# Kernel optimization log

Measured on AMD Instinct MI355X. Metric: run time of the kernel, lower is better.

Reference implementation:

```python
import jax, jax.numpy as jnp
import numpy as np

S_IN = 10.0   # sharpness_inside
S_OUT = 10.0  # sharpness_outside
NEG_FILL = -100.0  # value written outside the ellipsoid mask


def _quat_to_rot(q):
    # q: (B, M, 4) -> (B, M, 3, 3)
    q = q / jnp.linalg.norm(q, axis=-1, keepdims=True)
    w, x, y, z = q[..., 0], q[..., 1], q[..., 2], q[..., 3]
    R = jnp.stack([
        1 - 2 * (y * y + z * z), 2 * (x * y - w * z), 2 * (x * z + w * y),
        2 * (x * y + w * z), 1 - 2 * (x * x + z * z), 2 * (y * z - w * x),
        2 * (x * z - w * y), 2 * (y * z + w * x), 1 - 2 * (x * x + y * y),
    ], axis=-1)
    return R.reshape(q.shape[:-1] + (3, 3))


def setup_inputs() -> dict:
    key = jax.random.key(0)
    ks = jax.random.split(key, 12)
    B, N, P, M, C, H = 2, 256, 32, 16, 128, 256

    def lin(k, fan_in, shape):
        return (jax.random.normal(k, shape, jnp.float32) / np.sqrt(fan_in)).astype(jnp.float32)

    return {
        'ray_points': jax.random.normal(ks[0], (B, N, P, 3), jnp.float32),
        'translations': 0.5 * jax.random.normal(ks[1], (B, M, 3), jnp.float32),
        'rotations': jax.random.normal(ks[2], (B, M, 4), jnp.float32),
        'scale': 0.2 + 0.8 * jax.random.uniform(ks[3], (B, M, 3), jnp.float32),
        'part_shape_features': jax.random.normal(ks[4], (B, M, C), jnp.float32),
        'Wp': lin(ks[5], 3, (3, H)),   'bp': jnp.zeros((H,), jnp.float32),
        'Wc': lin(ks[6], C, (C, H)),   'bc': jnp.zeros((H,), jnp.float32),
        'W1': lin(ks[7], H, (H, H)),   'b1': jnp.zeros((H,), jnp.float32),
        'W2': lin(ks[8], H, (H, H)),   'b2': jnp.zeros((H,), jnp.float32),
        'Wout': lin(ks[9], H, (H, 1)), 'bout': jnp.zeros((1,), jnp.float32),
    }


def reference(ray_points, translations, rotations, scale, part_shape_features,
              Wp, bp, Wc, bc, W1, b1, W2, b2, Wout, bout):
    B, N, P, _ = ray_points.shape
    M = translations.shape[1]
    pts = ray_points.reshape(B, N * P, 3)

    # transform_to_primitives_centric_system: R @ (x - t)
    Xc = pts[:, :, None, :] - translations[:, None, :, :]          # (B, Np, M, 3)
    R = _quat_to_rot(rotations)                                    # (B, M, 3, 3)
    Xt = jnp.einsum('bmij,bnmj->bnmi', R, Xc)                      # (B, Np, M, 3)

    # inside_outside_function_ellipsoid: F = sum((x/a)^2)
    F_ell = jnp.sum((Xt / scale[:, None, :, :]) ** 2, axis=-1)     # (B, Np, M)
    mask = F_ell <= 1.0

    # MiniOccupancyNet: fc_p + per-block conditioning + resnet block + fc_out
    net = jnp.einsum('bnmd,dh->bnmh', Xt, Wp) + bp                 # (B, Np, M, H)
    cond = jnp.einsum('bmc,ch->bmh', part_shape_features, Wc) + bc # (B, M, H)
    net = net + cond[:, None, :, :]
    dx = jax.nn.relu(net) @ W1 + b1
    dx = jax.nn.relu(dx) @ W2 + b2
    net = net + dx
    occ = (jax.nn.relu(net) @ Wout + bout)[..., 0]                 # (B, Np, M)

    # masked gather-compute-scatter == dense compute + fill -100 outside mask
    F = jnp.where(mask, occ, NEG_FILL)

    # apply_sigmoid_to_inside_outside_function: piecewise sharpness
    sharp = jnp.where(F > 0, S_IN, S_OUT)
    implicit = jax.nn.sigmoid(sharp * F)                           # (B, Np, M)
    return implicit.reshape(B, N, P, M)
```

## Files before the change

### kernel.cpp

```cpp
#include <hip/hip_runtime.h>
#include <hip/hip_fp16.h>
#include <math.h>

#define B_   2
#define N_   256
#define P_   32
#define M_   16
#define C_   128
#define H_   256
#define NP_  (N_ * P_)
#define ROWS_ (B_ * NP_ * M_)
#define HALF_ (ROWS_ / 2)
#define TM_  64
#define LDA_ (H_ + 8)
#define MROWS_ 1024
#define MBLK_ (ROWS_ / MROWS_)

typedef _Float16 half8 __attribute__((ext_vector_type(8)));
typedef float f32x4 __attribute__((ext_vector_type(4)));

__global__ __launch_bounds__(256)
void prep_mask_k(const float* __restrict__ W1, const float* __restrict__ W2,
                 _Float16* __restrict__ Wt1, _Float16* __restrict__ Wt2,
                 const float* __restrict__ psf, const float* __restrict__ Wc,
                 const float* __restrict__ bc, const float* __restrict__ Wp,
                 const float* __restrict__ bp, _Float16* __restrict__ B0t,
                 const float* __restrict__ pts, const float* __restrict__ trans,
                 const float* __restrict__ rots, const float* __restrict__ scal,
                 int* __restrict__ cnt, int* __restrict__ wl,
                 float* __restrict__ out) {
    __shared__ float t[64][65];
    const int tid = threadIdx.x;

    if (blockIdx.x < 32) {
        const int id = blockIdx.x;
        const float* W = (id & 1) ? W2 : W1;
        _Float16* Wt = (id & 1) ? Wt2 : Wt1;
        const int tile = id >> 1, I = tile >> 2, J = tile & 3;
        const int r = tid >> 6, c = tid & 63;
        #pragma unroll
        for (int p = 0; p < 16; ++p)
            t[p * 4 + r][c] = W[(I * 64 + p * 4 + r) * H_ + J * 64 + c];
        __syncthreads();
        #pragma unroll
        for (int p = 0; p < 16; ++p)
            Wt[(J * 64 + p * 4 + r) * H_ + I * 64 + c] = (_Float16)t[c][p * 4 + r];
        return;
    }
    if (blockIdx.x < 64) {
        const int bm = blockIdx.x - 32;
        const int b = bm >> 4, m = bm & 15;
        const int h = tid;
        const float* p = psf + bm * C_;
        float acc = bc[h];
        for (int c = 0; c < C_; ++c) acc += p[c] * Wc[c * H_ + h];
        _Float16* dst = B0t + (b * H_ + h) * 32;
        dst[3 + m] = (_Float16)(acc + bp[h]);
        if (m == 0) {
            dst[0] = (_Float16)Wp[h];
            dst[1] = (_Float16)Wp[H_ + h];
            dst[2] = (_Float16)Wp[2 * H_ + h];
            #pragma unroll
            for (int k = 19; k < 32; ++k) dst[k] = (_Float16)0.0f;
        }
        return;
    }

    float (*sR)[9] = (float (*)[9])&t[0][0];
    float (*sT)[3] = (float (*)[3])&t[4][0];
    float (*sS)[3] = (float (*)[3])&t[8][0];
    __shared__ int sBuf[MROWS_];
    __shared__ int sCnt;
    __shared__ int sBase;

    const int base = (blockIdx.x - 64) * MROWS_;
    const int b    = base >> 17;

    if (tid == 0) sCnt = 0;
    if (tid < M_) {
        const int m = tid;
        const float* q = rots + (b * M_ + m) * 4;
        float w = q[0], x = q[1], y = q[2], z = q[3];
        float nrm = sqrtf(w * w + x * x + y * y + z * z);
        w /= nrm; x /= nrm; y /= nrm; z /= nrm;
        sR[m][0] = 1.0f - 2.0f * (y * y + z * z);
        sR[m][1] = 2.0f * (x * y - w * z);
        sR[m][2] = 2.0f * (x * z + w * y);
        sR[m][3] = 2.0f * (x * y + w * z);
        sR[m][4] = 1.0f - 2.0f * (x * x + z * z);
        sR[m][5] = 2.0f * (y * z - w * x);
        sR[m][6] = 2.0f * (x * z - w * y);
        sR[m][7] = 2.0f * (y * z + w * x);
        sR[m][8] = 1.0f - 2.0f * (x * x + y * y);
        const float* tp = trans + (b * M_ + m) * 3;
        sT[m][0] = tp[0]; sT[m][1] = tp[1]; sT[m][2] = tp[2];
        const float* sp = scal + (b * M_ + m) * 3;
        sS[m][0] = sp[0]; sS[m][1] = sp[1]; sS[m][2] = sp[2];
    }
    __syncthreads();

    const int m = tid & (M_ - 1);
    #pragma unroll
    for (int r = 0; r < 4; ++r) {
        const int row = base + r * 256 + tid;
        const int gp  = row >> 4;
        float fe;
        {
            #pragma clang fp contract(off)
            const float* p = pts + gp * 3;
            float x0 = p[0] - sT[m][0];
            float x1 = p[1] - sT[m][1];
            float x2 = p[2] - sT[m][2];
            float t0 = sR[m][0] * x0 + sR[m][1] * x1 + sR[m][2] * x2;
            float t1 = sR[m][3] * x0 + sR[m][4] * x1 + sR[m][5] * x2;
            float t2 = sR[m][6] * x0 + sR[m][7] * x1 + sR[m][8] * x2;
            float v0 = t0 / sS[m][0];
            float v1 = t1 / sS[m][1];
            float v2 = t2 / sS[m][2];
            fe = v0 * v0 + v1 * v1 + v2 * v2;
        }
        if (fe <= 1.0f) {
            const int pos = atomicAdd(&sCnt, 1);
            sBuf[pos] = row;
        } else {
            out[row] = 0.0f;
        }
    }
    __syncthreads();
    if (tid == 0) sBase = sCnt ? atomicAdd(&cnt[b], sCnt) : 0;
    __syncthreads();
    const int tot = sCnt, gb = b * HALF_ + sBase;
    for (int i = tid; i < tot; i += 256) wl[gb + i] = sBuf[i];
}

__global__ __launch_bounds__(256, 1)
void occ_k(const float* __restrict__ pts,  const float* __restrict__ trans,
           const float* __restrict__ rots, const float* __restrict__ scal,
           const float* __restrict__ b1v,  const float* __restrict__ b2v,
           const float* __restrict__ Wout, const float* __restrict__ bout,
           const _Float16* __restrict__ Wt1, const _Float16* __restrict__ Wt2,
           const _Float16* __restrict__ B0t, const int* __restrict__ cnt,
           const int* __restrict__ wl, float* __restrict__ out) {
    const int half = blockIdx.x >> 8;
    const int j0   = blockIdx.x & 255;
    const int count = cnt[half];
    if (j0 * TM_ >= count) return;

    __shared__ __align__(16) _Float16 sA0[TM_][32];
    __shared__ __align__(16) _Float16 sAbuf[TM_][LDA_];
    __shared__ float sR[M_][9];
    __shared__ float sT[M_][3];
    __shared__ float sS[M_][3];
    __shared__ float sPart[TM_][4];
    __shared__ int   sIdx[TM_];

    const int tid = threadIdx.x;
    const int b   = half;

    if (tid < M_) {
        const int m = tid;
        const float* q = rots + (b * M_ + m) * 4;
        float w = q[0], x = q[1], y = q[2], z = q[3];
        float nrm = sqrtf(w * w + x * x + y * y + z * z);
        w /= nrm; x /= nrm; y /= nrm; z /= nrm;
        sR[m][0] = 1.0f - 2.0f * (y * y + z * z);
        sR[m][1] = 2.0f * (x * y - w * z);
        sR[m][2] = 2.0f * (x * z + w * y);
        sR[m][3] = 2.0f * (x * y + w * z);
        sR[m][4] = 1.0f - 2.0f * (x * x + z * z);
        sR[m][5] = 2.0f * (y * z - w * x);
        sR[m][6] = 2.0f * (x * z - w * y);
        sR[m][7] = 2.0f * (y * z + w * x);
        sR[m][8] = 1.0f - 2.0f * (x * x + y * y);
        const float* tp = trans + (b * M_ + m) * 3;
        sT[m][0] = tp[0]; sT[m][1] = tp[1]; sT[m][2] = tp[2];
        const float* sp = scal + (b * M_ + m) * 3;
        sS[m][0] = sp[0]; sS[m][1] = sp[1]; sS[m][2] = sp[2];
    }

    const int w    = tid >> 6;
    const int lane = tid & 63;
    const int quad = lane >> 4;
    const int ln   = lane & 15;
    const f32x4 zero = {0.0f, 0.0f, 0.0f, 0.0f};

    for (int j = j0; j * TM_ < count; j += 256) {
        __syncthreads();
        if (tid < TM_) {
            const int k = j * TM_ + tid;
            sIdx[tid] = (k < count) ? wl[half * HALF_ + k] : -1;
        }
        __syncthreads();

        {
            const int r  = tid >> 2;
            const int kg = tid & 3;
            const int idx  = sIdx[r];
            const int safe = idx < 0 ? 0 : idx;
            const int m  = safe & (M_ - 1);
            const int gp = safe >> 4;
            half8 av;
            #pragma unroll
            for (int jj = 0; jj < 8; ++jj) av[jj] = (_Float16)0.0f;
            if (kg == 0) {
                float t0, t1, t2;
                {
                    #pragma clang fp contract(off)
                    const float* p = pts + gp * 3;
                    float x0 = p[0] - sT[m][0];
                    float x1 = p[1] - sT[m][1];
                    float x2 = p[2] - sT[m][2];
                    t0 = sR[m][0] * x0 + sR[m][1] * x1 + sR[m][2] * x2;
                    t1 = sR[m][3] * x0 + sR[m][4] * x1 + sR[m][5] * x2;
                    t2 = sR[m][6] * x0 + sR[m][7] * x1 + sR[m][8] * x2;
                }
                av[0] = (_Float16)t0; av[1] = (_Float16)t1; av[2] = (_Float16)t2;
                #pragma unroll
                for (int jj = 3; jj < 8; ++jj) av[jj] = (m == jj - 3) ? (_Float16)1.0f : (_Float16)0.0f;
            } else if (kg == 1) {
                #pragma unroll
                for (int jj = 0; jj < 8; ++jj) av[jj] = (m == 5 + jj) ? (_Float16)1.0f : (_Float16)0.0f;
            } else if (kg == 2) {
                #pragma unroll
                for (int jj = 0; jj < 3; ++jj) av[jj] = (m == 13 + jj) ? (_Float16)1.0f : (_Float16)0.0f;
            }
            *(half8*)&sA0[r][kg * 8] = av;
        }
        __syncthreads();

        f32x4 acc0[4][4];
        {
            half8 a0[4], b0[4];
            #pragma unroll
            for (int rt = 0; rt < 4; ++rt)
                a0[rt] = *(const half8*)&sA0[rt * 16 + ln][quad * 8];
            const _Float16* B0w = B0t + (b * H_ + w * 64) * 32 + quad * 8;
            #pragma unroll
            for (int tc = 0; tc < 4; ++tc)
                b0[tc] = *(const half8*)(B0w + (tc * 16 + ln) * 32);
            #pragma unroll
            for (int rt = 0; rt < 4; ++rt)
                #pragma unroll
                for (int tc = 0; tc < 4; ++tc)
                    acc0[rt][tc] = __builtin_amdgcn_mfma_f32_16x16x32_f16(a0[rt], b0[tc], zero, 0, 0, 0);

            #pragma unroll
            for (int tc = 0; tc < 4; ++tc) {
                const int col = w * 64 + tc * 16 + ln;
                #pragma unroll
                for (int rt = 0; rt < 4; ++rt)
                    #pragma unroll
                    for (int rg = 0; rg < 4; ++rg) {
                        float v = acc0[rt][tc][rg];
                        v = v > 0.0f ? v : 0.0f;
                        sAbuf[rt * 16 + quad * 4 + rg][col] = (_Float16)v;
                    }
            }
        }
        __syncthreads();

        f32x4 acc1[4][4];
        #pragma unroll
        for (int tc = 0; tc < 4; ++tc) {
            const float bb = b1v[w * 64 + tc * 16 + ln];
            const f32x4 bv = {bb, bb, bb, bb};
            #pragma unroll
            for (int rt = 0; rt < 4; ++rt) acc1[rt][tc] = bv;
        }
        {
            const _Float16* Wb1 = Wt1 + (w * 64) * H_;
            #pragma unroll
            for (int kc = 0; kc < 8; ++kc) {
                const int k0 = kc * 32 + quad * 8;
                half8 a[4], bf[4];
                #pragma unroll
                for (int rt = 0; rt < 4; ++rt)
                    a[rt] = *(const half8*)&sAbuf[rt * 16 + ln][k0];
                #pragma unroll
                for (int tc = 0; tc < 4; ++tc)
                    bf[tc] = *(const half8*)(Wb1 + (tc * 16 + ln) * H_ + k0);
                #pragma unroll
                for (int rt = 0; rt < 4; ++rt)
                    #pragma unroll
                    for (int tc = 0; tc < 4; ++tc)
                        acc1[rt][tc] = __builtin_amdgcn_mfma_f32_16x16x32_f16(a[rt], bf[tc], acc1[rt][tc], 0, 0, 0);
            }
        }
        __syncthreads();

        #pragma unroll
        for (int tc = 0; tc < 4; ++tc) {
            const int col = w * 64 + tc * 16 + ln;
            #pragma unroll
            for (int rt = 0; rt < 4; ++rt)
                #pragma unroll
                for (int rg = 0; rg < 4; ++rg) {
                    float v = acc1[rt][tc][rg];
                    v = v > 0.0f ? v : 0.0f;
                    sAbuf[rt * 16 + quad * 4 + rg][col] = (_Float16)v;
                }
        }
        __syncthreads();

        #pragma unroll
        for (int tc = 0; tc < 4; ++tc) {
            const float bb = b2v[w * 64 + tc * 16 + ln];
            const f32x4 bv = {bb, bb, bb, bb};
            #pragma unroll
            for (int rt = 0; rt < 4; ++rt) acc0[rt][tc] += bv;
        }
        {
            const _Float16* Wb2 = Wt2 + (w * 64) * H_;
            #pragma unroll
            for (int kc = 0; kc < 8; ++kc) {
                const int k0 = kc * 32 + quad * 8;
                half8 a[4], bf[4];
                #pragma unroll
                for (int rt = 0; rt < 4; ++rt)
                    a[rt] = *(const half8*)&sAbuf[rt * 16 + ln][k0];
                #pragma unroll
                for (int tc = 0; tc < 4; ++tc)
                    bf[tc] = *(const half8*)(Wb2 + (tc * 16 + ln) * H_ + k0);
                #pragma unroll
                for (int rt = 0; rt < 4; ++rt)
                    #pragma unroll
                    for (int tc = 0; tc < 4; ++tc)
                        acc0[rt][tc] = __builtin_amdgcn_mfma_f32_16x16x32_f16(a[rt], bf[tc], acc0[rt][tc], 0, 0, 0);
            }
        }

        float rowsum[4][4];
        #pragma unroll
        for (int rt = 0; rt < 4; ++rt)
            #pragma unroll
            for (int rg = 0; rg < 4; ++rg) rowsum[rt][rg] = 0.0f;

        #pragma unroll
        for (int tc = 0; tc < 4; ++tc) {
            const float wo = Wout[w * 64 + tc * 16 + ln];
            #pragma unroll
            for (int rt = 0; rt < 4; ++rt)
                #pragma unroll
                for (int rg = 0; rg < 4; ++rg) {
                    float net = acc0[rt][tc][rg];
                    net = net > 0.0f ? net : 0.0f;
                    rowsum[rt][rg] += net * wo;
                }
        }

        #pragma unroll
        for (int rt = 0; rt < 4; ++rt)
            #pragma unroll
            for (int rg = 0; rg < 4; ++rg) {
                float v = rowsum[rt][rg];
                v += __shfl_xor(v, 1, 16);
                v += __shfl_xor(v, 2, 16);
                v += __shfl_xor(v, 4, 16);
                v += __shfl_xor(v, 8, 16);
                if (ln == 0) sPart[rt * 16 + quad * 4 + rg][w] = v;
            }
        __syncthreads();

        if (tid < TM_) {
            const int idx = sIdx[tid];
            if (idx >= 0) {
                float occ = sPart[tid][0] + sPart[tid][1] + sPart[tid][2] + sPart[tid][3] + bout[0];
                out[idx] = 1.0f / (1.0f + __expf(-10.0f * occ));
            }
        }
    }
}

extern "C" void kernel_launch(void* const* d_in, const int* in_sizes, int n_in,
                              void* d_out, int out_size, void* d_ws, size_t ws_size,
                              hipStream_t stream) {
    const float* pts   = (const float*)d_in[0];
    const float* trans = (const float*)d_in[1];
    const float* rots  = (const float*)d_in[2];
    const float* scal  = (const float*)d_in[3];
    const float* psf   = (const float*)d_in[4];
    const float* Wp    = (const float*)d_in[5];
    const float* bp    = (const float*)d_in[6];
    const float* Wc    = (const float*)d_in[7];
    const float* bc    = (const float*)d_in[8];
    const float* W1    = (const float*)d_in[9];
    const float* b1    = (const float*)d_in[10];
    const float* W2    = (const float*)d_in[11];
    const float* b2    = (const float*)d_in[12];
    const float* Wout  = (const float*)d_in[13];
    const float* bout  = (const float*)d_in[14];
    float* out = (float*)d_out;

    char* ws = (char*)d_ws;
    _Float16* Wt1 = (_Float16*)ws;
    _Float16* Wt2 = (_Float16*)(ws + 131072);
    _Float16* B0t = (_Float16*)(ws + 262144);
    int*      cnt = (int*)(ws + 294912);
    int*      wl  = (int*)(ws + 295168);

    hipMemsetAsync(cnt, 0, 2 * sizeof(int), stream);
    hipLaunchKernelGGL(prep_mask_k, dim3(64 + MBLK_), dim3(256), 0, stream,
                       W1, W2, Wt1, Wt2, psf, Wc, bc, Wp, bp, B0t,
                       pts, trans, rots, scal, cnt, wl, out);
    hipLaunchKernelGGL(occ_k, dim3(512), dim3(256), 0, stream,
                       pts, trans, rots, scal, b1, b2, Wout, bout,
                       Wt1, Wt2, B0t, cnt, wl, out);
}
```

Before: 105.8 us.

## Fuse mask compaction into MLP kernel with per-block local worklists

The ellipsoid mask test and compaction move into the MLP kernel. Each block tests its own 1024 rows, compacts survivors in shared memory, and runs the MLP on them directly. This removes the memset, the global atomic worklist write and read, and one kernel boundary. In exchange, work per block now depends on how many of its rows survive, which can cause load imbalance across the 256 blocks.

Measured after the change: 117.0 us. +10.6%, slower.

```diff
diff --git a/kernel.cpp b/kernel.cpp
--- a/kernel.cpp
+++ b/kernel.cpp
@@ -10,7 +10,6 @@
 #define H_   256
 #define NP_  (N_ * P_)
 #define ROWS_ (B_ * NP_ * M_)
-#define HALF_ (ROWS_ / 2)
 #define TM_  64
 #define LDA_ (H_ + 8)
 #define MROWS_ 1024
@@ -20,18 +19,13 @@
 typedef float f32x4 __attribute__((ext_vector_type(4)));
 
 __global__ __launch_bounds__(256)
-void prep_mask_k(const float* __restrict__ W1, const float* __restrict__ W2,
-                 _Float16* __restrict__ Wt1, _Float16* __restrict__ Wt2,
-                 const float* __restrict__ psf, const float* __restrict__ Wc,
-                 const float* __restrict__ bc, const float* __restrict__ Wp,
-                 const float* __restrict__ bp, _Float16* __restrict__ B0t,
-                 const float* __restrict__ pts, const float* __restrict__ trans,
-                 const float* __restrict__ rots, const float* __restrict__ scal,
-                 int* __restrict__ cnt, int* __restrict__ wl,
-                 float* __restrict__ out) {
+void prep_k(const float* __restrict__ W1, const float* __restrict__ W2,
+            _Float16* __restrict__ Wt1, _Float16* __restrict__ Wt2,
+            const float* __restrict__ psf, const float* __restrict__ Wc,
+            const float* __restrict__ bc, const float* __restrict__ Wp,
+            const float* __restrict__ bp, _Float16* __restrict__ B0t) {
     __shared__ float t[64][65];
     const int tid = threadIdx.x;
-
     if (blockIdx.x < 32) {
         const int id = blockIdx.x;
         const float* W = (id & 1) ? W2 : W1;
@@ -45,9 +39,7 @@
         #pragma unroll
         for (int p = 0; p < 16; ++p)
             Wt[(J * 64 + p * 4 + r) * H_ + I * 64 + c] = (_Float16)t[c][p * 4 + r];
-        return;
-    }
-    if (blockIdx.x < 64) {
+    } else {
         const int bm = blockIdx.x - 32;
         const int b = bm >> 4, m = bm & 15;
         const int h = tid;
@@ -63,17 +55,27 @@
             #pragma unroll
             for (int k = 19; k < 32; ++k) dst[k] = (_Float16)0.0f;
         }
-        return;
     }
-
-    float (*sR)[9] = (float (*)[9])&t[0][0];
-    float (*sT)[3] = (float (*)[3])&t[4][0];
-    float (*sS)[3] = (float (*)[3])&t[8][0];
-    __shared__ int sBuf[MROWS_];
-    __shared__ int sCnt;
-    __shared__ int sBase;
-
-    const int base = (blockIdx.x - 64) * MROWS_;
+}
+
+__global__ __launch_bounds__(256, 1)
+void fused_k(const float* __restrict__ pts,  const float* __restrict__ trans,
+             const float* __restrict__ rots, const float* __restrict__ scal,
+             const float* __restrict__ b1v,  const float* __restrict__ b2v,
+             const float* __restrict__ Wout, const float* __restrict__ bout,
+             const _Float16* __restrict__ Wt1, const _Float16* __restrict__ Wt2,
+             const _Float16* __restrict__ B0t, float* __restrict__ out) {
+    __shared__ __align__(16) _Float16 sA0[TM_][32];
+    __shared__ __align__(16) _Float16 sAbuf[TM_][LDA_];
+    __shared__ float sR[M_][9];
+    __shared__ float sT[M_][3];
+    __shared__ float sS[M_][3];
+    __shared__ float sPart[TM_][4];
+    __shared__ int   sBuf[MROWS_];
+    __shared__ int   sCnt;
+
+    const int tid  = threadIdx.x;
+    const int base = blockIdx.x * MROWS_;
     const int b    = base >> 17;
 
     if (tid == 0) sCnt = 0;
@@ -99,84 +101,37 @@
     }
     __syncthreads();
 
-    const int m = tid & (M_ - 1);
-    #pragma unroll
-    for (int r = 0; r < 4; ++r) {
-        const int row = base + r * 256 + tid;
-        const int gp  = row >> 4;
-        float fe;
-        {
-            #pragma clang fp contract(off)
-            const float* p = pts + gp * 3;
-            float x0 = p[0] - sT[m][0];
-            float x1 = p[1] - sT[m][1];
-            float x2 = p[2] - sT[m][2];
-            float t0 = sR[m][0] * x0 + sR[m][1] * x1 + sR[m][2] * x2;
-            float t1 = sR[m][3] * x0 + sR[m][4] * x1 + sR[m][5] * x2;
-            float t2 = sR[m][6] * x0 + sR[m][7] * x1 + sR[m][8] * x2;
-            float v0 = t0 / sS[m][0];
-            float v1 = t1 / sS[m][1];
-            float v2 = t2 / sS[m][2];
-            fe = v0 * v0 + v1 * v1 + v2 * v2;
-        }
-        if (fe <= 1.0f) {
-            const int pos = atomicAdd(&sCnt, 1);
-            sBuf[pos] = row;
-        } else {
-            out[row] = 0.0f;
+    {
+        const int m = tid & (M_ - 1);
+        #pragma unroll
+        for (int r = 0; r < 4; ++r) {
+            const int row = base + r * 256 + tid;
+            const int gp  = row >> 4;
+            float fe;
+            {
+                #pragma clang fp contract(off)
+                const float* p = pts + gp * 3;
+                float x0 = p[0] - sT[m][0];
+                float x1 = p[1] - sT[m][1];
+                float x2 = p[2] - sT[m][2];
+                float t0 = sR[m][0] * x0 + sR[m][1] * x1 + sR[m][2] * x2;
+                float t1 = sR[m][3] * x0 + sR[m][4] * x1 + sR[m][5] * x2;
+                float t2 = sR[m][6] * x0 + sR[m][7] * x1 + sR[m][8] * x2;
+                float v0 = t0 / sS[m][0];
+                float v1 = t1 / sS[m][1];
+                float v2 = t2 / sS[m][2];
+                fe = v0 * v0 + v1 * v1 + v2 * v2;
+            }
+            if (fe <= 1.0f) {
+                const int pos = atomicAdd(&sCnt, 1);
+                sBuf[pos] = row;
+            } else {
+                out[row] = 0.0f;
+            }
         }
     }
     __syncthreads();
-    if (tid == 0) sBase = sCnt ? atomicAdd(&cnt[b], sCnt) : 0;
-    __syncthreads();
-    const int tot = sCnt, gb = b * HALF_ + sBase;
-    for (int i = tid; i < tot; i += 256) wl[gb + i] = sBuf[i];
-}
-
-__global__ __launch_bounds__(256, 1)
-void occ_k(const float* __restrict__ pts,  const float* __restrict__ trans,
-           const float* __restrict__ rots, const float* __restrict__ scal,
-           const float* __restrict__ b1v,  const float* __restrict__ b2v,
-           const float* __restrict__ Wout, const float* __restrict__ bout,
-           const _Float16* __restrict__ Wt1, const _Float16* __restrict__ Wt2,
-           const _Float16* __restrict__ B0t, const int* __restrict__ cnt,
-           const int* __restrict__ wl, float* __restrict__ out) {
-    const int half = blockIdx.x >> 8;
-    const int j0   = blockIdx.x & 255;
-    const int count = cnt[half];
-    if (j0 * TM_ >= count) return;
-
-    __shared__ __align__(16) _Float16 sA0[TM_][32];
-    __shared__ __align__(16) _Float16 sAbuf[TM_][LDA_];
-    __shared__ float sR[M_][9];
-    __shared__ float sT[M_][3];
-    __shared__ float sS[M_][3];
-    __shared__ float sPart[TM_][4];
-    __shared__ int   sIdx[TM_];
-
-    const int tid = threadIdx.x;
-    const int b   = half;
-
-    if (tid < M_) {
-        const int m = tid;
-        const float* q = rots + (b * M_ + m) * 4;
-        float w = q[0], x = q[1], y = q[2], z = q[3];
-        float nrm = sqrtf(w * w + x * x + y * y + z * z);
-        w /= nrm; x /= nrm; y /= nrm; z /= nrm;
-        sR[m][0] = 1.0f - 2.0f * (y * y + z * z);
-        sR[m][1] = 2.0f * (x * y - w * z);
-        sR[m][2] = 2.0f * (x * z + w * y);
-        sR[m][3] = 2.0f * (x * y + w * z);
-        sR[m][4] = 1.0f - 2.0f * (x * x + z * z);
-        sR[m][5] = 2.0f * (y * z - w * x);
-        sR[m][6] = 2.0f * (x * z - w * y);
-        sR[m][7] = 2.0f * (y * z + w * x);
-        sR[m][8] = 1.0f - 2.0f * (x * x + y * y);
-        const float* tp = trans + (b * M_ + m) * 3;
-        sT[m][0] = tp[0]; sT[m][1] = tp[1]; sT[m][2] = tp[2];
-        const float* sp = scal + (b * M_ + m) * 3;
-        sS[m][0] = sp[0]; sS[m][1] = sp[1]; sS[m][2] = sp[2];
-    }
+    const int count = sCnt;
 
     const int w    = tid >> 6;
     const int lane = tid & 63;
@@ -184,18 +139,12 @@
     const int ln   = lane & 15;
     const f32x4 zero = {0.0f, 0.0f, 0.0f, 0.0f};
 
-    for (int j = j0; j * TM_ < count; j += 256) {
-        __syncthreads();
-        if (tid < TM_) {
-            const int k = j * TM_ + tid;
-            sIdx[tid] = (k < count) ? wl[half * HALF_ + k] : -1;
-        }
-        __syncthreads();
-
+    for (int off = 0; off < count; off += TM_) {
         {
             const int r  = tid >> 2;
             const int kg = tid & 3;
-            const int idx  = sIdx[r];
+            const int k  = off + r;
+            const int idx  = (k < count) ? sBuf[k] : -1;
             const int safe = idx < 0 ? 0 : idx;
             const int m  = safe & (M_ - 1);
             const int gp = safe >> 4;
@@ -362,12 +311,14 @@
         __syncthreads();
 
         if (tid < TM_) {
-            const int idx = sIdx[tid];
-            if (idx >= 0) {
+            const int k = off + tid;
+            if (k < count) {
+                const int idx = sBuf[k];
                 float occ = sPart[tid][0] + sPart[tid][1] + sPart[tid][2] + sPart[tid][3] + bout[0];
                 out[idx] = 1.0f / (1.0f + __expf(-10.0f * occ));
             }
         }
+        __syncthreads();
     }
 }
 
@@ -395,14 +346,10 @@
     _Float16* Wt1 = (_Float16*)ws;
     _Float16* Wt2 = (_Float16*)(ws + 131072);
     _Float16* B0t = (_Float16*)(ws + 262144);
-    int*      cnt = (int*)(ws + 294912);
-    int*      wl  = (int*)(ws + 295168);
-
-    hipMemsetAsync(cnt, 0, 2 * sizeof(int), stream);
-    hipLaunchKernelGGL(prep_mask_k, dim3(64 + MBLK_), dim3(256), 0, stream,
-                       W1, W2, Wt1, Wt2, psf, Wc, bc, Wp, bp, B0t,
-                       pts, trans, rots, scal, cnt, wl, out);
-    hipLaunchKernelGGL(occ_k, dim3(512), dim3(256), 0, stream,
+
+    hipLaunchKernelGGL(prep_k, dim3(64), dim3(256), 0, stream,
+                       W1, W2, Wt1, Wt2, psf, Wc, bc, Wp, bp, B0t);
+    hipLaunchKernelGGL(fused_k, dim3(MBLK_), dim3(256), 0, stream,
                        pts, trans, rots, scal, b1, b2, Wout, bout,
-                       Wt1, Wt2, B0t, cnt, wl, out);
+                       Wt1, Wt2, B0t, out);
 }
```
